# Kernel optimization log

Measured on AMD Instinct MI355X. Metric: run time of the kernel, lower is better.

The kernel has to match this reference:

```python
import jax, jax.numpy as jnp
import numpy as np

# loss weights / thresholds (match module defaults)
L_RC, L_HU, L_EDGE, L_TEX = 2.0, 1.5, 1.0, 0.8
L_HF, L_SYN, L_IC, L_MID, L_LF = 1.5, 1.0, 0.8, 0.8, 0.6
MIN_BODY, ART_FACTOR, FLAT_TH = 4096, 2.0, 0.03

SOBEL_X = jnp.array([[-1., 0., 1.], [-2., 0., 2.], [-1., 0., 1.]], jnp.float32)
SOBEL_Y = jnp.array([[-1., -2., -1.], [0., 0., 0.], [1., 2., 1.]], jnp.float32)
LAP = jnp.array([[0., 1., 0.], [1., -4., 1.], [0., 1., 0.]], jnp.float32)

def _conv2d(x, k):
    # x: (B,1,H,W), k: (kh,kw), 'same' padding single-channel conv
    kh, kw = k.shape
    return jax.lax.conv_general_dilated(
        x, k[None, None].astype(x.dtype), (1, 1),
        [(kh // 2, kh // 2), (kw // 2, kw // 2)],
        dimension_numbers=('NCHW', 'OIHW', 'NCHW'))

def _gauss_kernel(sigma):
    k = int(6 * sigma + 1)
    if k % 2 == 0:
        k += 1
    c = jnp.arange(k, dtype=jnp.float32) - k // 2
    g = jnp.exp(-0.5 * (c / sigma) ** 2)
    g = g / g.sum()
    return g[:, None] * g[None, :]

def _masked_mean(x, mask):
    cnt = jnp.sum(mask)
    return jnp.sum(jnp.where(mask, x, 0.0)) / jnp.maximum(cnt, 1)

def _masked_l1(a, b, mask):
    cnt = jnp.sum(mask)
    return jnp.sum(jnp.where(mask, jnp.abs(a - b), 0.0)) / jnp.maximum(cnt, 1)

def _masked_quantile(x, mask, q):
    # torch.quantile(x[mask], q) with linear interpolation
    v = jnp.sort(jnp.where(mask, x, jnp.inf).ravel())
    n = jnp.maximum(jnp.sum(mask), 1)
    pos = q * (n - 1).astype(x.dtype)
    lo = jnp.clip(jnp.floor(pos).astype(jnp.int32), 0, v.size - 1)
    hi = jnp.clip(jnp.ceil(pos).astype(jnp.int32), 0, v.size - 1)
    frac = pos - lo.astype(x.dtype)
    return v[lo] * (1.0 - frac) + v[hi] * frac

def setup_inputs() -> dict:
    key = jax.random.key(0)
    ks = jax.random.split(key, 7)
    B, H, W = 16, 768, 768
    return {
        'y_pred': jax.random.uniform(ks[0], (B, 1, 1, H, W), jnp.float32),
        'noise_pred': jax.random.normal(ks[1], (B, 1, 1, H, W), jnp.float32),
        'x_i': jax.random.uniform(ks[2], (B, 1, H, W), jnp.float32),
        'x_ip1': jax.random.uniform(ks[3], (B, 1, H, W), jnp.float32),
        'x_mid': jax.random.uniform(ks[4], (B, 1, H, W), jnp.float32),
        'W': jax.random.uniform(ks[5], (B, 1, H, W), jnp.float32),
        'noise_synthetic': jax.random.normal(ks[6], (B, 1, H, W), jnp.float32),
    }

def reference(y_pred, noise_pred, x_i, x_ip1, x_mid, W, noise_synthetic):
    yp = y_pred[:, :, 0]          # (B,1,H,W)
    npred = noise_pred[:, :, 0]

    # reconstruction
    loss_rc = jnp.mean(jnp.abs(yp * W - x_i * W))

    # HU consistency on body mask
    body = (x_i > 0.15) & (x_i < 0.85)
    nb = jnp.sum(body)
    mean_in = _masked_mean(x_i, body)
    mean_pr = _masked_mean(yp, body)
    hu = (mean_pr - mean_in) ** 2 + 0.5 * (
        (_masked_quantile(yp, body, 0.25) - _masked_quantile(x_i, body, 0.25)) ** 2
        + (_masked_quantile(yp, body, 0.75) - _masked_quantile(x_i, body, 0.75)) ** 2)
    loss_hu = jnp.where(nb > MIN_BODY, hu, 0.0)

    # edges
    gxp, gyp = _conv2d(yp, SOBEL_X), _conv2d(yp, SOBEL_Y)
    gxi, gyi = _conv2d(x_i, SOBEL_X), _conv2d(x_i, SOBEL_Y)
    loss_edge = jnp.mean(jnp.abs(gxp - gxi)) + jnp.mean(jnp.abs(gyp - gyi))

    gmi = jnp.sqrt(gxi ** 2 + gyi ** 2 + 1e-8)
    gmp = jnp.sqrt(gxp ** 2 + gyp ** 2 + 1e-8)

    # texture
    tex = (gmi > FLAT_TH) & (gmi < 0.5)
    loss_texture = jnp.where(jnp.sum(tex) > 100, _masked_l1(gmp, gmi, tex), 0.0)

    flat = gmi < FLAT_TH
    fb = flat & body
    nfb = jnp.sum(fb)

    # low/mid frequency losses on flat body regions
    G3, G1 = _gauss_kernel(3.0), _gauss_kernel(1.0)
    low_i, low_p, low_m = _conv2d(x_i, G3), _conv2d(yp, G3), _conv2d(x_mid, G3)
    lf = _masked_l1(low_p - low_m, 0.3 * (low_i - low_m), fb)
    mid_i = _conv2d(x_i, G1) - low_i
    mid_p = _conv2d(yp, G1) - low_p
    mid = _masked_l1(jnp.abs(mid_p), 0.3 * jnp.abs(mid_i), fb)
    loss_lf = jnp.where(nfb > 100, lf, 0.0)
    loss_mid = jnp.where(nfb > 100, mid, 0.0)

    # high-frequency noise via laplacian on flat regions
    lap_i, lap_p = _conv2d(x_i, LAP), _conv2d(yp, LAP)
    nf = jnp.sum(flat)
    loss_hf = jnp.where(nf > 100, _masked_l1(jnp.abs(lap_p), 0.3 * jnp.abs(lap_i), flat), 0.0)

    # synthetic noise supervision on flat body
    loss_syn = jnp.where(nfb > 100, _masked_l1(npred, noise_synthetic, fb), 0.0)

    # artifact penalty on flat regions
    ic = _masked_mean(jnp.maximum(gmp - ART_FACTOR * gmi, 0.0), flat)
    loss_ic = jnp.where(nf > 100, ic, 0.0)

    total = (L_RC * loss_rc + L_HU * loss_hu + L_EDGE * loss_edge
             + L_TEX * loss_texture + L_HF * loss_hf + L_MID * loss_mid
             + L_LF * loss_lf + L_SYN * loss_syn + L_IC * loss_ic)
    return total
```

## Files before the change

kernel.cpp:

```cpp
#include <hip/hip_runtime.h>


#define HH 768
#define WW 768
#define BB 16
#define HWSZ (HH * WW)
#define NPXD ((double)BB * (double)HWSZ)

#define NB 1024
#define NHIST (2 * NB)

#define STRIPS 3
#define HSEG 12
#define NSEG (HH / HSEG)
#define NJOBS (STRIPS * NSEG * BB)
#define NBLK1 (NJOBS / 4)

#define FBBUF 128

__device__ __forceinline__ float wredf(float v) {
#pragma unroll
  for (int o = 32; o > 0; o >>= 1) v += __shfl_down(v, o, 64);
  return v;
}
__device__ __forceinline__ unsigned wredu(unsigned v) {
#pragma unroll
  for (int o = 32; o > 0; o >>= 1) v += __shfl_down(v, o, 64);
  return v;
}

struct Row {
  float f[4];
  float l, r;
};

__device__ __forceinline__ Row load_row(const float* __restrict__ p, int y,
                                        int xl, int x0, int lane) {
  Row r;
  if (y < 0 || y >= HH) {
    r.f[0] = r.f[1] = r.f[2] = r.f[3] = 0.f;
    r.l = 0.f;
    r.r = 0.f;
    return r;
  }
  const float4 v = *(const float4*)(p + (size_t)y * WW + xl);
  r.f[0] = v.x; r.f[1] = v.y; r.f[2] = v.z; r.f[3] = v.w;
  float left = __shfl_up(v.w, 1, 64);
  float right = __shfl_down(v.x, 1, 64);
  if (lane == 0) left = (x0 > 0) ? p[(size_t)y * WW + x0 - 1] : 0.f;
  if (lane == 63) right = (x0 + 256 < WW) ? p[(size_t)y * WW + x0 + 256] : 0.f;
  r.l = left;
  r.r = right;
  return r;
}

#define LNB(row, j) ((j) == 0 ? (row).l : (row).f[(j)-1])
#define RNB(row, j) ((j) == 3 ? (row).r : (row).f[(j) + 1])


__global__ __launch_bounds__(256) void pass1_kernel(
    const float* __restrict__ yp, const float* __restrict__ xi,
    const float* __restrict__ wt, double* __restrict__ accs,
    unsigned* __restrict__ cnts, unsigned* __restrict__ fb_list, int fb_cap,
    unsigned* __restrict__ hist_final) {
  __shared__ unsigned s_hist[NHIST];
  __shared__ unsigned s_fb[4][FBBUF];
  __shared__ unsigned s_fbn[4];
  __shared__ float s_redf[4][8];
  __shared__ unsigned s_redc[4][3];

  const int tid = threadIdx.x;
  const int lane = tid & 63;
  const int wv = tid >> 6;
  const unsigned long long lmask_lt = (1ull << lane) - 1ull;

  for (int i = tid; i < NHIST; i += 256) s_hist[i] = 0u;
  if (lane == 0) s_fbn[wv] = 0u;
  __syncthreads();

  const int job = blockIdx.x * 4 + wv;
  const int s = job % STRIPS;
  const int seg = (job / STRIPS) % NSEG;
  const int b = job / (STRIPS * NSEG);
  const int x0 = s * 256;
  const int y0 = seg * HSEG;
  const int xl = x0 + lane * 4;
  const size_t base = (size_t)b * HWSZ;
  const float* ypb = yp + base;
  const float* xib = xi + base;
  const float* wtb = wt + base;

  float a_rc = 0.f, a_sxi = 0.f, a_syp = 0.f, a_ex = 0.f, a_ey = 0.f;
  float a_tex = 0.f, a_hf = 0.f, a_ic = 0.f;
  unsigned c_body = 0u, c_tex = 0u, c_flat = 0u;

  Row pm1 = load_row(ypb, y0 - 1, xl, x0, lane);
  Row pc = load_row(ypb, y0, xl, x0, lane);
  Row im1 = load_row(xib, y0 - 1, xl, x0, lane);
  Row icr = load_row(xib, y0, xl, x0, lane);

  for (int y = y0; y < y0 + HSEG; y++) {
    const Row pp1 = load_row(ypb, y + 1, xl, x0, lane);
    const Row ip1 = load_row(xib, y + 1, xl, x0, lane);
    const float4 w4 = *(const float4*)(wtb + (size_t)y * WW + xl);
    const float wf[4] = {w4.x, w4.y, w4.z, w4.w};

#pragma unroll
    for (int j = 0; j < 4; j++) {
      const float p00 = LNB(pm1, j), p01 = pm1.f[j], p02 = RNB(pm1, j);
      const float p10 = LNB(pc, j),  p11 = pc.f[j],  p12 = RNB(pc, j);
      const float p20 = LNB(pp1, j), p21 = pp1.f[j], p22 = RNB(pp1, j);
      const float i00 = LNB(im1, j), i01 = im1.f[j], i02 = RNB(im1, j);
      const float i10 = LNB(icr, j), i11 = icr.f[j], i12 = RNB(icr, j);
      const float i20 = LNB(ip1, j), i21 = ip1.f[j], i22 = RNB(ip1, j);

      const float gxp = (p02 - p00) + 2.f * (p12 - p10) + (p22 - p20);
      const float gyp = (p20 - p00) + 2.f * (p21 - p01) + (p22 - p02);
      const float lapp = p01 + p10 + p12 + p21 - 4.f * p11;
      const float gxi_ = (i02 - i00) + 2.f * (i12 - i10) + (i22 - i20);
      const float gyi_ = (i20 - i00) + 2.f * (i21 - i01) + (i22 - i02);
      const float lapi = i01 + i10 + i12 + i21 - 4.f * i11;

      const float yv = p11, xv = i11;
      a_rc += fabsf(yv * wf[j] - xv * wf[j]);

      const bool body = (xv > 0.15f) && (xv < 0.85f);
      if (body) {
        c_body++;
        a_sxi += xv;
        a_syp += yv;
        int bx = (int)(xv * (float)NB);
        bx = bx < 0 ? 0 : (bx > NB - 1 ? NB - 1 : bx);
        int by = (int)(yv * (float)NB);
        by = by < 0 ? 0 : (by > NB - 1 ? NB - 1 : by);
        atomicAdd(&s_hist[bx], 1u);
        atomicAdd(&s_hist[NB + by], 1u);
      }

      a_ex += fabsf(gxp - gxi_);
      a_ey += fabsf(gyp - gyi_);

      const float gmi = sqrtf(gxi_ * gxi_ + gyi_ * gyi_ + 1e-8f);
      const float gmp = sqrtf(gxp * gxp + gyp * gyp + 1e-8f);

      if (gmi > 0.03f && gmi < 0.5f) {
        c_tex++;
        a_tex += fabsf(gmp - gmi);
      }
      const bool flat = gmi < 0.03f;
      if (flat) {
        c_flat++;
        a_hf += fabsf(fabsf(lapp) - 0.3f * fabsf(lapi));
        a_ic += fmaxf(gmp - 2.0f * gmi, 0.f);
      }
      const bool qual = flat && body;
      const unsigned long long m = __ballot(qual);
      if (m) {
        const unsigned bofs = s_fbn[wv];
        if (qual) {
          const unsigned p = bofs + (unsigned)__popcll(m & lmask_lt);
          const unsigned gidx = (unsigned)(base + (size_t)y * WW + (xl + j));
          if (p < FBBUF) {
            s_fb[wv][p] = gidx;
          } else {
            const unsigned gi = atomicAdd(&cnts[3], 1u);
            if ((int)gi < fb_cap) fb_list[gi] = gidx;
          }
        }
        s_fbn[wv] = bofs + (unsigned)__popcll(m);
      }
    }
    pm1 = pc; pc = pp1;
    im1 = icr; icr = ip1;
  }

  {
    unsigned n = s_fbn[wv];
    if (n > FBBUF) n = FBBUF;
    unsigned gbase = 0u;
    if (lane == 0 && n > 0) gbase = atomicAdd(&cnts[3], n);
    gbase = __shfl(gbase, 0, 64);
    for (unsigned i = lane; i < n; i += 64) {
      const unsigned gi = gbase + i;
      if ((int)gi < fb_cap) fb_list[gi] = s_fb[wv][i];
    }
  }

  __syncthreads();
  for (int i = tid; i < NHIST; i += 256) {
    const unsigned v = s_hist[i];
    if (v) atomicAdd(&hist_final[i], v);
  }

  float f0 = wredf(a_rc), f1 = wredf(a_sxi), f2 = wredf(a_syp);
  float f3 = wredf(a_ex), f4 = wredf(a_ey), f5 = wredf(a_tex);
  float f6 = wredf(a_hf), f7 = wredf(a_ic);
  unsigned u0 = wredu(c_body), u1 = wredu(c_tex), u2 = wredu(c_flat);
  if (lane == 0) {
    s_redf[wv][0] = f0; s_redf[wv][1] = f1; s_redf[wv][2] = f2; s_redf[wv][3] = f3;
    s_redf[wv][4] = f4; s_redf[wv][5] = f5; s_redf[wv][6] = f6; s_redf[wv][7] = f7;
    s_redc[wv][0] = u0; s_redc[wv][1] = u1; s_redc[wv][2] = u2;
  }
  __syncthreads();
  if (tid < 8) {
    double sm = (double)s_redf[0][tid] + (double)s_redf[1][tid] +
                (double)s_redf[2][tid] + (double)s_redf[3][tid];
    atomicAdd(&accs[tid], sm);
  } else if (tid < 11) {
    int k = tid - 8;
    unsigned sm = s_redc[0][k] + s_redc[1][k] + s_redc[2][k] + s_redc[3][k];
    atomicAdd(&cnts[k], sm);
  }
}

__global__ __launch_bounds__(256) void pass2_kernel(
    const float* __restrict__ yp, const float* __restrict__ xi,
    const float* __restrict__ xm, const float* __restrict__ npred,
    const float* __restrict__ nsyn, double* __restrict__ accs,
    const unsigned* __restrict__ cnts, const unsigned* __restrict__ fb_list,
    int fb_cap) {
  __shared__ float w3[19];
  __shared__ float w1[7];
  __shared__ double s_red[4][3];
  const int tid = threadIdx.x;
  const int lane = tid & 63;
  const int wv = tid >> 6;

  if (tid == 0) {
    float tmp[19], s = 0.f;
    for (int i = 0; i < 19; i++) {
      float c = (float)(i - 9) / 3.0f;
      tmp[i] = expf(-0.5f * c * c);
      s += tmp[i];
    }
    for (int i = 0; i < 19; i++) w3[i] = tmp[i] / s;
    float tmp1[7], s1 = 0.f;
    for (int i = 0; i < 7; i++) {
      float c = (float)(i - 3);
      tmp1[i] = expf(-0.5f * c * c);
      s1 += tmp1[i];
    }
    for (int i = 0; i < 7; i++) w1[i] = tmp1[i] / s1;
  }
  __syncthreads();

  unsigned nfb = cnts[3];
  if (nfb > (unsigned)fb_cap) nfb = (unsigned)fb_cap;
  const int wid = (int)((blockIdx.x * blockDim.x + tid) >> 6);
  const int nwaves = (int)((gridDim.x * blockDim.x) >> 6);

  double w_lf = 0.0, w_md = 0.0, w_sy = 0.0;

  for (int i = wid; i < (int)nfb; i += nwaves) {
    const unsigned px = fb_list[i];
    const int b = (int)(px / (unsigned)HWSZ);
    const int rem = (int)(px % (unsigned)HWSZ);
    const int y = rem / WW;
    const int x = rem % WW;
    const size_t base = (size_t)b * HWSZ;
    const float* xib = xi + base;
    const float* ypb = yp + base;
    const float* xmb = xm + base;

    float npv = 0.f, nsv = 0.f;
    if (lane == 0) { npv = npred[px]; nsv = nsyn[px]; }

    float s_li = 0.f, s_lp = 0.f, s_lm = 0.f;
    float s_gi = 0.f, s_gp = 0.f;
    const bool interior = (y >= 9) && (y < HH - 9) && (x >= 9) && (x < WW - 9);
    if (interior) {
#pragma unroll
      for (int k = 0; k < 6; k++) {
        const int tap = lane + 64 * k;
        if (tap < 361) {
          const int r = tap / 19, c = tap - r * 19;
          const float wgt = w3[r] * w3[c];
          const int o = (y + r - 9) * WW + (x + c - 9);
          s_li += wgt * xib[o];
          s_lp += wgt * ypb[o];
          s_lm += wgt * xmb[o];
        }
      }
      if (lane < 49) {
        const int r = lane / 7, c = lane - r * 7;
        const float wgt = w1[r] * w1[c];
        const int o = (y + r - 3) * WW + (x + c - 3);
        s_gi = wgt * xib[o];
        s_gp = wgt * ypb[o];
      }
    } else {
#pragma unroll
      for (int k = 0; k < 6; k++) {
        const int tap = lane + 64 * k;
        if (tap < 361) {
          const int r = tap / 19, c = tap - r * 19;
          const int gy = y + r - 9, gx = x + c - 9;
          if (gy >= 0 && gy < HH && gx >= 0 && gx < WW) {
            const float wgt = w3[r] * w3[c];
            const int o = gy * WW + gx;
            s_li += wgt * xib[o];
            s_lp += wgt * ypb[o];
            s_lm += wgt * xmb[o];
          }
        }
      }
      if (lane < 49) {
        const int r = lane / 7, c = lane - r * 7;
        const int gy = y + r - 3, gx = x + c - 3;
        if (gy >= 0 && gy < HH && gx >= 0 && gx < WW) {
          const float wgt = w1[r] * w1[c];
          const int o = gy * WW + gx;
          s_gi = wgt * xib[o];
          s_gp = wgt * ypb[o];
        }
      }
    }
    s_li = wredf(s_li);
    s_lp = wredf(s_lp);
    s_lm = wredf(s_lm);
    s_gi = wredf(s_gi);
    s_gp = wredf(s_gp);
    if (lane == 0) {
      const float lf = fabsf((s_lp - s_lm) - 0.3f * (s_li - s_lm));
      const float mi_ = s_gi - s_li, mp_ = s_gp - s_lp;
      const float md = fabsf(fabsf(mp_) - 0.3f * fabsf(mi_));
      w_lf += (double)lf;
      w_md += (double)md;
      w_sy += (double)fabsf(npv - nsv);
    }
  }

  if (lane == 0) {
    s_red[wv][0] = w_lf; s_red[wv][1] = w_md; s_red[wv][2] = w_sy;
  }
  __syncthreads();
  if (tid < 3) {
    const double t = s_red[0][tid] + s_red[1][tid] + s_red[2][tid] + s_red[3][tid];
    if (t != 0.0) atomicAdd(&accs[8 + tid], t);
  }
}

__global__ __launch_bounds__(256) void finalize_kernel(
    const double* __restrict__ accs, const unsigned* __restrict__ cnts,
    const unsigned* __restrict__ hist, float* __restrict__ out) {
  __shared__ unsigned sc[NHIST];
  __shared__ unsigned wsum[8];
  __shared__ double quant[4];
  const int tid = threadIdx.x;
  const int lane = tid & 63;
  const int wv = tid >> 6;

  if (tid < 4) quant[tid] = 0.0;

#pragma unroll
  for (int h = 0; h < 2; h++) {
    const int baseh = h * NB + tid * 4;
    const unsigned v0 = hist[baseh + 0];
    const unsigned v1 = hist[baseh + 1];
    const unsigned v2 = hist[baseh + 2];
    const unsigned v3 = hist[baseh + 3];
    const unsigned s = v0 + v1 + v2 + v3;
    unsigned scl = s;
#pragma unroll
    for (int o = 1; o < 64; o <<= 1) {
      const unsigned t = __shfl_up(scl, o, 64);
      if (lane >= o) scl += t;
    }
    if (lane == 63) wsum[h * 4 + wv] = scl;
    __syncthreads();
    unsigned woff = 0;
    for (int k = 0; k < wv; k++) woff += wsum[h * 4 + k];
    const unsigned excl = woff + scl - s;
    const unsigned c0 = excl + v0;
    const unsigned c1 = c0 + v1;
    const unsigned c2 = c1 + v2;
    const unsigned c3 = c2 + v3;
    sc[baseh + 0] = c0;
    sc[baseh + 1] = c1;
    sc[baseh + 2] = c2;
    sc[baseh + 3] = c3;
    __syncthreads();
  }

  const unsigned nb = cnts[0];
  if (tid < 4 && nb > 4096u) {
    const int h = tid >> 1;
    const double q = (tid & 1) ? 0.75 : 0.25;
    const double pos = q * (double)(nb - 1u);
    int lo = 0, hi = NB - 1;
    while (lo < hi) {
      const int mid = (lo + hi) >> 1;
      if ((double)sc[h * NB + mid] > pos) hi = mid; else lo = mid + 1;
    }
    const unsigned cum_before = (lo > 0) ? sc[h * NB + lo - 1] : 0u;
    const unsigned m = sc[h * NB + lo] - cum_before;
    const double local = pos - (double)cum_before;
    quant[tid] = ((double)lo + (local + 0.5) / (double)(m ? m : 1u)) *
                 (1.0 / (double)NB);
  }
  __syncthreads();
  if (tid != 0) return;

  const unsigned ntex = cnts[1], nflat = cnts[2], nfb = cnts[3];
  const double loss_rc = accs[0] / NPXD;
  const double denb = (double)(nb > 0u ? nb : 1u);
  const double mean_in = accs[1] / denb;
  const double mean_pr = accs[2] / denb;

  double loss_hu = 0.0;
  if (nb > 4096u) {
    const double q25i = quant[0], q75i = quant[1];
    const double q25p = quant[2], q75p = quant[3];
    const double d = mean_pr - mean_in;
    loss_hu = d * d + 0.5 * ((q25p - q25i) * (q25p - q25i) +
                             (q75p - q75i) * (q75p - q75i));
  }

  const double loss_edge = accs[3] / NPXD + accs[4] / NPXD;
  const double loss_tex = (ntex > 100u) ? accs[5] / (double)(ntex ? ntex : 1u) : 0.0;
  const double loss_hf = (nflat > 100u) ? accs[6] / (double)(nflat ? nflat : 1u) : 0.0;
  const double loss_ic = (nflat > 100u) ? accs[7] / (double)(nflat ? nflat : 1u) : 0.0;
  const double denfb = (double)(nfb > 0u ? nfb : 1u);
  const double loss_lf = (nfb > 100u) ? accs[8] / denfb : 0.0;
  const double loss_mid = (nfb > 100u) ? accs[9] / denfb : 0.0;
  const double loss_syn = (nfb > 100u) ? accs[10] / denfb : 0.0;

  const double total = 2.0 * loss_rc + 1.5 * loss_hu + 1.0 * loss_edge +
                       0.8 * loss_tex + 1.5 * loss_hf + 0.8 * loss_mid +
                       0.6 * loss_lf + 1.0 * loss_syn + 0.8 * loss_ic;
  out[0] = (float)total;
}

extern "C" void kernel_launch(void* const* d_in, const int* in_sizes, int n_in,
                              void* d_out, int out_size, void* d_ws,
                              size_t ws_size, hipStream_t stream) {
  (void)in_sizes; (void)n_in; (void)out_size;
  const float* y_pred = (const float*)d_in[0];
  const float* noise_pred = (const float*)d_in[1];
  const float* x_i = (const float*)d_in[2];
  const float* x_mid = (const float*)d_in[4];
  const float* Wt = (const float*)d_in[5];
  const float* nsyn = (const float*)d_in[6];
  float* out = (float*)d_out;

  char* ws = (char*)d_ws;
  double* accs = (double*)ws;
  unsigned* cnts = (unsigned*)(ws + 128);
  unsigned* hist_final = (unsigned*)(ws + 256);
  const size_t FIXED = 16384;

  size_t avail = (ws_size > FIXED) ? (ws_size - FIXED) : 0;
  long long cap = (long long)(avail / 4);
  if (cap > (long long)BB * HWSZ) cap = (long long)BB * HWSZ;
  int fb_cap = (int)cap;
  unsigned* fb_list = (unsigned*)(ws + FIXED);

  hipMemsetAsync(ws, 0, FIXED, stream);
  pass1_kernel<<<NBLK1, 256, 0, stream>>>(y_pred, x_i, Wt, accs, cnts,
                                          fb_list, fb_cap, hist_final);
  pass2_kernel<<<256, 256, 0, stream>>>(y_pred, x_i, x_mid, noise_pred, nsyn,
                                        accs, cnts, fb_list, fb_cap);
  finalize_kernel<<<1, 256, 0, stream>>>(accs, cnts, hist_final, out);
}
```

Measured before the change: 261.9 us.

## Fuse three passes into one cooperative kernel with grid syncs

Merges pass1, pass2 and finalize into a single cooperative launch with grid-wide syncs, halves the row segment height so the grid doubles to 1536 blocks, and spreads histogram atomics over 8 copies that finalize sums. The aim is to remove launch gaps between kernels and reduce atomic contention on the global histogram. The cooperative launch needs every block resident at once (6 blocks/CU bound). If that launch fails the code falls back to the separate kernels, and more of the shared pass2 list work now runs on the larger grid.

```diff
diff --git a/kernel.cpp b/kernel.cpp
--- a/kernel.cpp
+++ b/kernel.cpp
@@ -1,4 +1,7 @@
 #include <hip/hip_runtime.h>
+#include <hip/hip_cooperative_groups.h>
+
+namespace cg = cooperative_groups;
 
 
 #define HH 768
@@ -9,12 +12,13 @@
 
 #define NB 1024
 #define NHIST (2 * NB)
+#define NCOPY 8
 
 #define STRIPS 3
-#define HSEG 12
-#define NSEG (HH / HSEG)
-#define NJOBS (STRIPS * NSEG * BB)
-#define NBLK1 (NJOBS / 4)
+#define F_HSEG 6
+#define F_NSEG (HH / F_HSEG)
+#define F_NJOBS (STRIPS * F_NSEG * BB)
+#define F_NBLK (F_NJOBS / 4)
 
 #define FBBUF 128
 
@@ -58,32 +62,21 @@
 #define RNB(row, j) ((j) == 3 ? (row).r : (row).f[(j) + 1])
 
 
-__global__ __launch_bounds__(256) void pass1_kernel(
+__device__ __forceinline__ void pass1_work(
     const float* __restrict__ yp, const float* __restrict__ xi,
     const float* __restrict__ wt, double* __restrict__ accs,
     unsigned* __restrict__ cnts, unsigned* __restrict__ fb_list, int fb_cap,
-    unsigned* __restrict__ hist_final) {
-  __shared__ unsigned s_hist[NHIST];
-  __shared__ unsigned s_fb[4][FBBUF];
-  __shared__ unsigned s_fbn[4];
-  __shared__ float s_redf[4][8];
-  __shared__ unsigned s_redc[4][3];
-
-  const int tid = threadIdx.x;
-  const int lane = tid & 63;
-  const int wv = tid >> 6;
+    unsigned* __restrict__ hist_final, unsigned (&s_hist)[NHIST],
+    unsigned (&s_fb)[4][FBBUF], unsigned (&s_fbn)[4], float (&s_redf)[4][8],
+    unsigned (&s_redc)[4][3], int tid, int lane, int wv) {
   const unsigned long long lmask_lt = (1ull << lane) - 1ull;
-
-  for (int i = tid; i < NHIST; i += 256) s_hist[i] = 0u;
-  if (lane == 0) s_fbn[wv] = 0u;
-  __syncthreads();
 
   const int job = blockIdx.x * 4 + wv;
   const int s = job % STRIPS;
-  const int seg = (job / STRIPS) % NSEG;
-  const int b = job / (STRIPS * NSEG);
+  const int seg = (job / STRIPS) % F_NSEG;
+  const int b = job / (STRIPS * F_NSEG);
   const int x0 = s * 256;
-  const int y0 = seg * HSEG;
+  const int y0 = seg * F_HSEG;
   const int xl = x0 + lane * 4;
   const size_t base = (size_t)b * HWSZ;
   const float* ypb = yp + base;
@@ -99,7 +92,7 @@
   Row im1 = load_row(xib, y0 - 1, xl, x0, lane);
   Row icr = load_row(xib, y0, xl, x0, lane);
 
-  for (int y = y0; y < y0 + HSEG; y++) {
+  for (int y = y0; y < y0 + F_HSEG; y++) {
     const Row pp1 = load_row(ypb, y + 1, xl, x0, lane);
     const Row ip1 = load_row(xib, y + 1, xl, x0, lane);
     const float4 w4 = *(const float4*)(wtb + (size_t)y * WW + xl);
@@ -164,7 +157,9 @@
             s_fb[wv][p] = gidx;
           } else {
             const unsigned gi = atomicAdd(&cnts[3], 1u);
-            if ((int)gi < fb_cap) fb_list[gi] = gidx;
+            if ((int)gi < fb_cap)
+              __hip_atomic_store(&fb_list[gi], gidx, __ATOMIC_RELAXED,
+                                 __HIP_MEMORY_SCOPE_AGENT);
           }
         }
         s_fbn[wv] = bofs + (unsigned)__popcll(m);
@@ -182,14 +177,19 @@
     gbase = __shfl(gbase, 0, 64);
     for (unsigned i = lane; i < n; i += 64) {
       const unsigned gi = gbase + i;
-      if ((int)gi < fb_cap) fb_list[gi] = s_fb[wv][i];
+      if ((int)gi < fb_cap)
+        __hip_atomic_store(&fb_list[gi], s_fb[wv][i], __ATOMIC_RELAXED,
+                           __HIP_MEMORY_SCOPE_AGENT);
     }
   }
 
   __syncthreads();
-  for (int i = tid; i < NHIST; i += 256) {
-    const unsigned v = s_hist[i];
-    if (v) atomicAdd(&hist_final[i], v);
+  {
+    const unsigned hco = ((unsigned)blockIdx.x & (NCOPY - 1)) * NHIST;
+    for (int i = tid; i < NHIST; i += 256) {
+      const unsigned v = s_hist[i];
+      if (v) atomicAdd(&hist_final[hco + i], v);
+    }
   }
 
   float f0 = wredf(a_rc), f1 = wredf(a_sxi), f2 = wredf(a_syp);
@@ -213,46 +213,22 @@
   }
 }
 
-__global__ __launch_bounds__(256) void pass2_kernel(
+__device__ __forceinline__ void pass2_work(
     const float* __restrict__ yp, const float* __restrict__ xi,
     const float* __restrict__ xm, const float* __restrict__ npred,
     const float* __restrict__ nsyn, double* __restrict__ accs,
     const unsigned* __restrict__ cnts, const unsigned* __restrict__ fb_list,
-    int fb_cap) {
-  __shared__ float w3[19];
-  __shared__ float w1[7];
-  __shared__ double s_red[4][3];
-  const int tid = threadIdx.x;
-  const int lane = tid & 63;
-  const int wv = tid >> 6;
-
-  if (tid == 0) {
-    float tmp[19], s = 0.f;
-    for (int i = 0; i < 19; i++) {
-      float c = (float)(i - 9) / 3.0f;
-      tmp[i] = expf(-0.5f * c * c);
-      s += tmp[i];
-    }
-    for (int i = 0; i < 19; i++) w3[i] = tmp[i] / s;
-    float tmp1[7], s1 = 0.f;
-    for (int i = 0; i < 7; i++) {
-      float c = (float)(i - 3);
-      tmp1[i] = expf(-0.5f * c * c);
-      s1 += tmp1[i];
-    }
-    for (int i = 0; i < 7; i++) w1[i] = tmp1[i] / s1;
-  }
-  __syncthreads();
-
-  unsigned nfb = cnts[3];
+    int fb_cap, const float (&w3)[19], const float (&w1)[7],
+    double (&s_red)[4][3], int tid, int lane, int wv, int wid, int nwaves) {
+  unsigned nfb =
+      __hip_atomic_load(&cnts[3], __ATOMIC_RELAXED, __HIP_MEMORY_SCOPE_AGENT);
   if (nfb > (unsigned)fb_cap) nfb = (unsigned)fb_cap;
-  const int wid = (int)((blockIdx.x * blockDim.x + tid) >> 6);
-  const int nwaves = (int)((gridDim.x * blockDim.x) >> 6);
 
   double w_lf = 0.0, w_md = 0.0, w_sy = 0.0;
 
   for (int i = wid; i < (int)nfb; i += nwaves) {
-    const unsigned px = fb_list[i];
+    const unsigned px = __hip_atomic_load(&fb_list[i], __ATOMIC_RELAXED,
+                                          __HIP_MEMORY_SCOPE_AGENT);
     const int b = (int)(px / (unsigned)HWSZ);
     const int rem = (int)(px % (unsigned)HWSZ);
     const int y = rem / WW;
@@ -335,30 +311,31 @@
   }
   __syncthreads();
   if (tid < 3) {
-    const double t = s_red[0][tid] + s_red[1][tid] + s_red[2][tid] + s_red[3][tid];
+    const double t =
+        s_red[0][tid] + s_red[1][tid] + s_red[2][tid] + s_red[3][tid];
     if (t != 0.0) atomicAdd(&accs[8 + tid], t);
   }
 }
 
-__global__ __launch_bounds__(256) void finalize_kernel(
+__device__ __forceinline__ void finalize_work(
     const double* __restrict__ accs, const unsigned* __restrict__ cnts,
-    const unsigned* __restrict__ hist, float* __restrict__ out) {
-  __shared__ unsigned sc[NHIST];
-  __shared__ unsigned wsum[8];
-  __shared__ double quant[4];
-  const int tid = threadIdx.x;
-  const int lane = tid & 63;
-  const int wv = tid >> 6;
-
+    const unsigned* __restrict__ hist, float* __restrict__ out,
+    unsigned (&sc)[NHIST], unsigned (&wsum)[8], double (&quant)[4], int tid,
+    int lane, int wv) {
   if (tid < 4) quant[tid] = 0.0;
 
 #pragma unroll
   for (int h = 0; h < 2; h++) {
     const int baseh = h * NB + tid * 4;
-    const unsigned v0 = hist[baseh + 0];
-    const unsigned v1 = hist[baseh + 1];
-    const unsigned v2 = hist[baseh + 2];
-    const unsigned v3 = hist[baseh + 3];
+    unsigned v0 = 0u, v1 = 0u, v2 = 0u, v3 = 0u;
+#pragma unroll
+    for (int c = 0; c < NCOPY; c++) {
+      const unsigned* hb = hist + c * NHIST + baseh;
+      v0 += __hip_atomic_load(&hb[0], __ATOMIC_RELAXED, __HIP_MEMORY_SCOPE_AGENT);
+      v1 += __hip_atomic_load(&hb[1], __ATOMIC_RELAXED, __HIP_MEMORY_SCOPE_AGENT);
+      v2 += __hip_atomic_load(&hb[2], __ATOMIC_RELAXED, __HIP_MEMORY_SCOPE_AGENT);
+      v3 += __hip_atomic_load(&hb[3], __ATOMIC_RELAXED, __HIP_MEMORY_SCOPE_AGENT);
+    }
     const unsigned s = v0 + v1 + v2 + v3;
     unsigned scl = s;
 #pragma unroll
@@ -382,7 +359,8 @@
     __syncthreads();
   }
 
-  const unsigned nb = cnts[0];
+  const unsigned nb =
+      __hip_atomic_load(&cnts[0], __ATOMIC_RELAXED, __HIP_MEMORY_SCOPE_AGENT);
   if (tid < 4 && nb > 4096u) {
     const int h = tid >> 1;
     const double q = (tid & 1) ? 0.75 : 0.25;
@@ -399,36 +377,179 @@
                  (1.0 / (double)NB);
   }
   __syncthreads();
-  if (tid != 0) return;
-
-  const unsigned ntex = cnts[1], nflat = cnts[2], nfb = cnts[3];
-  const double loss_rc = accs[0] / NPXD;
-  const double denb = (double)(nb > 0u ? nb : 1u);
-  const double mean_in = accs[1] / denb;
-  const double mean_pr = accs[2] / denb;
-
-  double loss_hu = 0.0;
-  if (nb > 4096u) {
-    const double q25i = quant[0], q75i = quant[1];
-    const double q25p = quant[2], q75p = quant[3];
-    const double d = mean_pr - mean_in;
-    loss_hu = d * d + 0.5 * ((q25p - q25i) * (q25p - q25i) +
-                             (q75p - q75i) * (q75p - q75i));
-  }
-
-  const double loss_edge = accs[3] / NPXD + accs[4] / NPXD;
-  const double loss_tex = (ntex > 100u) ? accs[5] / (double)(ntex ? ntex : 1u) : 0.0;
-  const double loss_hf = (nflat > 100u) ? accs[6] / (double)(nflat ? nflat : 1u) : 0.0;
-  const double loss_ic = (nflat > 100u) ? accs[7] / (double)(nflat ? nflat : 1u) : 0.0;
-  const double denfb = (double)(nfb > 0u ? nfb : 1u);
-  const double loss_lf = (nfb > 100u) ? accs[8] / denfb : 0.0;
-  const double loss_mid = (nfb > 100u) ? accs[9] / denfb : 0.0;
-  const double loss_syn = (nfb > 100u) ? accs[10] / denfb : 0.0;
-
-  const double total = 2.0 * loss_rc + 1.5 * loss_hu + 1.0 * loss_edge +
-                       0.8 * loss_tex + 1.5 * loss_hf + 0.8 * loss_mid +
-                       0.6 * loss_lf + 1.0 * loss_syn + 0.8 * loss_ic;
-  out[0] = (float)total;
+  if (tid == 0) {
+    const unsigned ntex = __hip_atomic_load(&cnts[1], __ATOMIC_RELAXED,
+                                            __HIP_MEMORY_SCOPE_AGENT);
+    const unsigned nflat = __hip_atomic_load(&cnts[2], __ATOMIC_RELAXED,
+                                             __HIP_MEMORY_SCOPE_AGENT);
+    const unsigned nfb = __hip_atomic_load(&cnts[3], __ATOMIC_RELAXED,
+                                           __HIP_MEMORY_SCOPE_AGENT);
+    double A[11];
+#pragma unroll
+    for (int i = 0; i < 11; i++)
+      A[i] = __hip_atomic_load(&accs[i], __ATOMIC_RELAXED,
+                               __HIP_MEMORY_SCOPE_AGENT);
+
+    const double loss_rc = A[0] / NPXD;
+    const double denb = (double)(nb > 0u ? nb : 1u);
+    const double mean_in = A[1] / denb;
+    const double mean_pr = A[2] / denb;
+
+    double loss_hu = 0.0;
+    if (nb > 4096u) {
+      const double q25i = quant[0], q75i = quant[1];
+      const double q25p = quant[2], q75p = quant[3];
+      const double d = mean_pr - mean_in;
+      loss_hu = d * d + 0.5 * ((q25p - q25i) * (q25p - q25i) +
+                               (q75p - q75i) * (q75p - q75i));
+    }
+
+    const double loss_edge = A[3] / NPXD + A[4] / NPXD;
+    const double loss_tex =
+        (ntex > 100u) ? A[5] / (double)(ntex ? ntex : 1u) : 0.0;
+    const double loss_hf =
+        (nflat > 100u) ? A[6] / (double)(nflat ? nflat : 1u) : 0.0;
+    const double loss_ic =
+        (nflat > 100u) ? A[7] / (double)(nflat ? nflat : 1u) : 0.0;
+    const double denfb = (double)(nfb > 0u ? nfb : 1u);
+    const double loss_lf = (nfb > 100u) ? A[8] / denfb : 0.0;
+    const double loss_mid = (nfb > 100u) ? A[9] / denfb : 0.0;
+    const double loss_syn = (nfb > 100u) ? A[10] / denfb : 0.0;
+
+    const double total = 2.0 * loss_rc + 1.5 * loss_hu + 1.0 * loss_edge +
+                         0.8 * loss_tex + 1.5 * loss_hf + 0.8 * loss_mid +
+                         0.6 * loss_lf + 1.0 * loss_syn + 0.8 * loss_ic;
+    out[0] = (float)total;
+  }
+}
+
+__global__ __launch_bounds__(256, 6) void fused_kernel(
+    const float* __restrict__ yp, const float* __restrict__ xi,
+    const float* __restrict__ wt, const float* __restrict__ xm,
+    const float* __restrict__ npred, const float* __restrict__ nsyn,
+    double* __restrict__ accs, unsigned* __restrict__ cnts,
+    unsigned* __restrict__ fb_list, int fb_cap,
+    unsigned* __restrict__ hist_final, float* __restrict__ out) {
+  __shared__ unsigned s_hist[NHIST];
+  __shared__ unsigned s_fb[4][FBBUF];
+  __shared__ unsigned s_fbn[4];
+  __shared__ float s_redf[4][8];
+  __shared__ unsigned s_redc[4][3];
+  __shared__ float w3[19];
+  __shared__ float w1[7];
+  __shared__ double s_red2[4][3];
+  __shared__ unsigned wsum[8];
+  __shared__ double quant[4];
+
+  const int tid = threadIdx.x;
+  const int lane = tid & 63;
+  const int wv = tid >> 6;
+
+  for (int i = tid; i < NHIST; i += 256) s_hist[i] = 0u;
+  if (lane == 0) s_fbn[wv] = 0u;
+  if (tid == 0) {
+    float tmp[19], s = 0.f;
+    for (int i = 0; i < 19; i++) {
+      float c = (float)(i - 9) / 3.0f;
+      tmp[i] = expf(-0.5f * c * c);
+      s += tmp[i];
+    }
+    for (int i = 0; i < 19; i++) w3[i] = tmp[i] / s;
+    float tmp1[7], s1 = 0.f;
+    for (int i = 0; i < 7; i++) {
+      float c = (float)(i - 3);
+      tmp1[i] = expf(-0.5f * c * c);
+      s1 += tmp1[i];
+    }
+    for (int i = 0; i < 7; i++) w1[i] = tmp1[i] / s1;
+  }
+  __syncthreads();
+
+  pass1_work(yp, xi, wt, accs, cnts, fb_list, fb_cap, hist_final, s_hist,
+             s_fb, s_fbn, s_redf, s_redc, tid, lane, wv);
+
+  cg::this_grid().sync();
+
+  {
+    const int wid = (int)(blockIdx.x * 4 + wv);
+    const int nwaves = F_NBLK * 4;
+    pass2_work(yp, xi, xm, npred, nsyn, accs, cnts, fb_list, fb_cap, w3, w1,
+               s_red2, tid, lane, wv, wid, nwaves);
+  }
+
+  cg::this_grid().sync();
+
+  if (blockIdx.x == 0) {
+    finalize_work(accs, cnts, hist_final, out, s_hist, wsum, quant, tid, lane,
+                  wv);
+  }
+}
+
+__global__ __launch_bounds__(256, 6) void pass1_kernel(
+    const float* __restrict__ yp, const float* __restrict__ xi,
+    const float* __restrict__ wt, double* __restrict__ accs,
+    unsigned* __restrict__ cnts, unsigned* __restrict__ fb_list, int fb_cap,
+    unsigned* __restrict__ hist_final) {
+  __shared__ unsigned s_hist[NHIST];
+  __shared__ unsigned s_fb[4][FBBUF];
+  __shared__ unsigned s_fbn[4];
+  __shared__ float s_redf[4][8];
+  __shared__ unsigned s_redc[4][3];
+  const int tid = threadIdx.x;
+  const int lane = tid & 63;
+  const int wv = tid >> 6;
+  for (int i = tid; i < NHIST; i += 256) s_hist[i] = 0u;
+  if (lane == 0) s_fbn[wv] = 0u;
+  __syncthreads();
+  pass1_work(yp, xi, wt, accs, cnts, fb_list, fb_cap, hist_final, s_hist,
+             s_fb, s_fbn, s_redf, s_redc, tid, lane, wv);
+}
+
+__global__ __launch_bounds__(256) void pass2_kernel(
+    const float* __restrict__ yp, const float* __restrict__ xi,
+    const float* __restrict__ xm, const float* __restrict__ npred,
+    const float* __restrict__ nsyn, double* __restrict__ accs,
+    const unsigned* __restrict__ cnts, const unsigned* __restrict__ fb_list,
+    int fb_cap) {
+  __shared__ float w3[19];
+  __shared__ float w1[7];
+  __shared__ double s_red2[4][3];
+  const int tid = threadIdx.x;
+  const int lane = tid & 63;
+  const int wv = tid >> 6;
+  if (tid == 0) {
+    float tmp[19], s = 0.f;
+    for (int i = 0; i < 19; i++) {
+      float c = (float)(i - 9) / 3.0f;
+      tmp[i] = expf(-0.5f * c * c);
+      s += tmp[i];
+    }
+    for (int i = 0; i < 19; i++) w3[i] = tmp[i] / s;
+    float tmp1[7], s1 = 0.f;
+    for (int i = 0; i < 7; i++) {
+      float c = (float)(i - 3);
+      tmp1[i] = expf(-0.5f * c * c);
+      s1 += tmp1[i];
+    }
+    for (int i = 0; i < 7; i++) w1[i] = tmp1[i] / s1;
+  }
+  __syncthreads();
+  const int wid = (int)((blockIdx.x * blockDim.x + tid) >> 6);
+  const int nwaves = (int)((gridDim.x * blockDim.x) >> 6);
+  pass2_work(yp, xi, xm, npred, nsyn, accs, cnts, fb_list, fb_cap, w3, w1,
+             s_red2, tid, lane, wv, wid, nwaves);
+}
+
+__global__ __launch_bounds__(256) void finalize_kernel(
+    const double* __restrict__ accs, const unsigned* __restrict__ cnts,
+    const unsigned* __restrict__ hist, float* __restrict__ out) {
+  __shared__ unsigned sc[NHIST];
+  __shared__ unsigned wsum[8];
+  __shared__ double quant[4];
+  const int tid = threadIdx.x;
+  const int lane = tid & 63;
+  const int wv = tid >> 6;
+  finalize_work(accs, cnts, hist, out, sc, wsum, quant, tid, lane, wv);
 }
 
 extern "C" void kernel_launch(void* const* d_in, const int* in_sizes, int n_in,
@@ -447,7 +568,7 @@
   double* accs = (double*)ws;
   unsigned* cnts = (unsigned*)(ws + 128);
   unsigned* hist_final = (unsigned*)(ws + 256);
-  const size_t FIXED = 16384;
+  const size_t FIXED = 256 + (size_t)NCOPY * NHIST * 4;
 
   size_t avail = (ws_size > FIXED) ? (ws_size - FIXED) : 0;
   long long cap = (long long)(avail / 4);
@@ -456,9 +577,29 @@
   unsigned* fb_list = (unsigned*)(ws + FIXED);
 
   hipMemsetAsync(ws, 0, FIXED, stream);
-  pass1_kernel<<<NBLK1, 256, 0, stream>>>(y_pred, x_i, Wt, accs, cnts,
-                                          fb_list, fb_cap, hist_final);
-  pass2_kernel<<<256, 256, 0, stream>>>(y_pred, x_i, x_mid, noise_pred, nsyn,
-                                        accs, cnts, fb_list, fb_cap);
-  finalize_kernel<<<1, 256, 0, stream>>>(accs, cnts, hist_final, out);
-}
+
+  void* kargs[12];
+  kargs[0] = (void*)&y_pred;
+  kargs[1] = (void*)&x_i;
+  kargs[2] = (void*)&Wt;
+  kargs[3] = (void*)&x_mid;
+  kargs[4] = (void*)&noise_pred;
+  kargs[5] = (void*)&nsyn;
+  kargs[6] = (void*)&accs;
+  kargs[7] = (void*)&cnts;
+  kargs[8] = (void*)&fb_list;
+  kargs[9] = (void*)&fb_cap;
+  kargs[10] = (void*)&hist_final;
+  kargs[11] = (void*)&out;
+
+  hipError_t err = hipLaunchCooperativeKernel(
+      (const void*)fused_kernel, dim3(F_NBLK), dim3(256), kargs, 0, stream);
+  if (err != hipSuccess) {
+    (void)hipGetLastError();
+    pass1_kernel<<<F_NBLK, 256, 0, stream>>>(y_pred, x_i, Wt, accs, cnts,
+                                             fb_list, fb_cap, hist_final);
+    pass2_kernel<<<256, 256, 0, stream>>>(y_pred, x_i, x_mid, noise_pred,
+                                          nsyn, accs, cnts, fb_list, fb_cap);
+    finalize_kernel<<<1, 256, 0, stream>>>(accs, cnts, hist_final, out);
+  }
+}
```

After: 667.7 us. 155% more time.
